# Performance work log

Measured on AMD Instinct MI355X. Metric: run time of the kernel, lower is better.

## Reference

```python
import jax, jax.numpy as jnp
import numpy as np

D_MODEL = 1024
N_HEADS = 16
D_HEAD = D_MODEL // N_HEADS
B, S = 4, 2048
NEG_INF = float('-inf')


def setup_inputs() -> dict:
    key = jax.random.key(0)
    ks = jax.random.split(key, 12)
    sc = 1.0 / np.sqrt(D_MODEL)
    inp = {
        'query': jax.random.normal(ks[0], (B, S, D_MODEL), jnp.float32),
        'key': jax.random.normal(ks[1], (B, S, D_MODEL), jnp.float32),
        'value': jax.random.normal(ks[2], (B, S, D_MODEL), jnp.float32),
        'mask': jnp.ones((B, S), jnp.int32),
        'W_q': jax.random.normal(ks[3], (D_MODEL, D_MODEL), jnp.float32) * sc,
        'b_q': jax.random.normal(ks[4], (D_MODEL,), jnp.float32) * sc,
        'W_k': jax.random.normal(ks[5], (D_MODEL, D_MODEL), jnp.float32) * sc,
        'b_k': jax.random.normal(ks[6], (D_MODEL,), jnp.float32) * sc,
        'W_v': jax.random.normal(ks[7], (D_MODEL, D_MODEL), jnp.float32) * sc,
        'b_v': jax.random.normal(ks[8], (D_MODEL,), jnp.float32) * sc,
        'W_o': jax.random.normal(ks[9], (D_MODEL, D_MODEL), jnp.float32) * sc,
        'b_o': jax.random.normal(ks[10], (D_MODEL,), jnp.float32) * sc,
    }
    return inp


def reference(query, key, value, mask, W_q, b_q, W_k, b_k, W_v, b_v, W_o, b_o):
    b, s, d = query.shape
    # QKV projections, split heads: [B,S,D] -> [B,H,S,Dh]
    def proj(x, W, bias):
        y = x @ W + bias
        return y.reshape(b, s, N_HEADS, D_HEAD).transpose(0, 2, 1, 3)
    q = proj(query, W_q, b_q)
    k = proj(key, W_k, b_k)
    v = proj(value, W_v, b_v)
    # NOTE: original scales by d_head**2 (not sqrt) — kept faithful.
    e = jnp.einsum('bhqd,bhkd->bhqk', q, k) / (D_HEAD ** 2)
    # key padding mask: [B,S] -> additive [B,1,1,S]
    pad = jnp.where(mask == 0, NEG_INF, 0.0).astype(e.dtype)[:, None, None, :]
    e = e + pad
    # causal mask: additive lower-triangular
    causal = jnp.where(jnp.tril(jnp.ones((s, s), bool)), 0.0, NEG_INF).astype(e.dtype)
    e = e + causal[None, None, :, :]
    a = jax.nn.softmax(e, axis=-1)
    c = jnp.einsum('bhqk,bhkd->bhqd', a, v)  # [B,H,S,Dh]
    c = c.transpose(0, 2, 1, 3).reshape(b, s, d)
    return c @ W_o + b_o
```

## Files before the change

### kernel.cpp

```cpp
#include <hip/hip_runtime.h>

typedef __bf16 bf16;
typedef unsigned int u32;
typedef float f32x4 __attribute__((ext_vector_type(4)));
typedef __bf16 bf16x4 __attribute__((ext_vector_type(4)));
typedef __bf16 bf16x8 __attribute__((ext_vector_type(8)));

#define MFMA(a, b, c) __builtin_amdgcn_mfma_f32_16x16x32_bf16((a), (b), (c), 0, 0, 0)

static constexpr int Bc = 4;
static constexpr int Sc = 2048;
static constexpr int Hc = 16;
static constexpr int DHc = 64;
static constexpr int Dc = 1024;
static constexpr int Mc = Bc * Sc;

__device__ __forceinline__ void load_lds16(const bf16* gp, bf16* lp) {
    __builtin_amdgcn_global_load_lds(
        reinterpret_cast<const __attribute__((address_space(1))) u32*>(
            reinterpret_cast<uintptr_t>(gp)),
        reinterpret_cast<__attribute__((address_space(3))) u32*>(
            static_cast<u32>(reinterpret_cast<uintptr_t>(lp))),
        16, 0, 0);
}

__global__ void fill_diag(float* out, int n) {
    int i = blockIdx.x * 256 + threadIdx.x;
    if (i < n) out[i] = 1000.0f;
}

__global__ __launch_bounds__(256) void cvt_bf16(const float* __restrict__ in,
                                                bf16* __restrict__ out, int n) {
    int i = (blockIdx.x * 256 + threadIdx.x) * 8;
    if (i < n) {
        f32x4 a = *(const f32x4*)&in[i];
        f32x4 b = *(const f32x4*)&in[i + 4];
        bf16x8 v;
#pragma unroll
        for (int j = 0; j < 4; ++j) { v[j] = (bf16)a[j]; v[j + 4] = (bf16)b[j]; }
        *(bf16x8*)&out[i] = v;
    }
}

__global__ __launch_bounds__(256) void transpose4(
    const float* __restrict__ A0, const float* __restrict__ A1,
    const float* __restrict__ A2, const float* __restrict__ A3,
    bf16* __restrict__ O0, bf16* __restrict__ O1,
    bf16* __restrict__ O2, bf16* __restrict__ O3) {
    __shared__ bf16 t[32][33];
    const float* in = blockIdx.z == 0 ? A0 : blockIdx.z == 1 ? A1
                    : blockIdx.z == 2 ? A2 : A3;
    bf16* out = blockIdx.z == 0 ? O0 : blockIdx.z == 1 ? O1
              : blockIdx.z == 2 ? O2 : O3;
    int x = blockIdx.x * 32 + threadIdx.x;
#pragma unroll
    for (int j = 0; j < 32; j += 8) {
        int y = blockIdx.y * 32 + threadIdx.y + j;
        t[threadIdx.y + j][threadIdx.x] = (bf16)in[y * 1024 + x];
    }
    __syncthreads();
    int x2 = blockIdx.y * 32 + threadIdx.x;
#pragma unroll
    for (int j = 0; j < 32; j += 8) {
        int y2 = blockIdx.x * 32 + threadIdx.y + j;
        out[y2 * 1024 + x2] = t[threadIdx.x][threadIdx.y + j];
    }
}

template <int MODE, typename TOUT>
__global__ __launch_bounds__(256) void gemm_bt(const bf16* __restrict__ A,
                                               const bf16* __restrict__ Wt,
                                               const float* __restrict__ bias,
                                               TOUT* __restrict__ out,
                                               int M, int N, int K) {
    __shared__ alignas(16) bf16 As[128 * 32];
    __shared__ alignas(16) bf16 Bs[128 * 32];
    const int tid = threadIdx.x;
    const int wave = tid >> 6, lane = tid & 63;
    const int quad = lane >> 4, l16 = lane & 15;
    const int wr = (wave >> 1) * 64, wc = (wave & 1) * 64;
    const int id = blockIdx.y * 8 + blockIdx.x;
    const int sw = (id & 7) * 64 + (id >> 3);
    const int row0 = (sw >> 3) * 128, col0 = (sw & 7) * 128;

    const int sr = wave * 32 + (lane >> 2);
    const int sk = (lane & 3) * 8;
    const bf16* gA = &A[(size_t)(row0 + sr) * K + sk];
    const bf16* gB = &Wt[(size_t)(col0 + sr) * K + sk];
    bf16* lA = &As[wave * 32 * 32];
    bf16* lB = &Bs[wave * 32 * 32];

    f32x4 acc[4][4];
#pragma unroll
    for (int mi = 0; mi < 4; ++mi)
#pragma unroll
        for (int ni = 0; ni < 4; ++ni)
            acc[mi][ni] = (f32x4){0.f, 0.f, 0.f, 0.f};

    for (int k0 = 0; k0 < K; k0 += 32) {
        __syncthreads();
        load_lds16(gA + k0, lA);
        load_lds16(gA + k0 + 16 * K, lA + 16 * 32);
        load_lds16(gB + k0, lB);
        load_lds16(gB + k0 + 16 * K, lB + 16 * 32);
        __syncthreads();

        bf16x8 af[4], bf_[4];
#pragma unroll
        for (int mi = 0; mi < 4; ++mi)
            af[mi] = *(const bf16x8*)&As[(wr + mi * 16 + l16) * 32 + quad * 8];
#pragma unroll
        for (int ni = 0; ni < 4; ++ni)
            bf_[ni] = *(const bf16x8*)&Bs[(wc + ni * 16 + l16) * 32 + quad * 8];
#pragma unroll
        for (int mi = 0; mi < 4; ++mi)
#pragma unroll
            for (int ni = 0; ni < 4; ++ni)
                acc[mi][ni] = MFMA(af[mi], bf_[ni], acc[mi][ni]);
    }

#pragma unroll
    for (int mi = 0; mi < 4; ++mi) {
#pragma unroll
        for (int ni = 0; ni < 4; ++ni) {
            int col = col0 + wc + ni * 16 + l16;
            float bv = bias[col];
#pragma unroll
            for (int r = 0; r < 4; ++r) {
                int row = row0 + wr + mi * 16 + quad * 4 + r;
                float v = acc[mi][ni][r] + bv;
                size_t off;
                if (MODE == 0) {
                    off = (size_t)row * N + col;
                } else {
                    int b = row >> 11, s = row & (Sc - 1);
                    int h = col >> 6, dh = col & (DHc - 1);
                    if (MODE == 1)
                        off = (((size_t)(b * Hc + h) * Sc + s) << 6) + dh;
                    else
                        off = (((size_t)(b * Hc + h) * DHc + dh) << 11) + s;
                }
                out[off] = (TOUT)v;
            }
        }
    }
}

static constexpr int LPP = 72;
static constexpr float CEXP = 1.4426950408889634f / 4096.0f;

__global__ __launch_bounds__(256, 2) void attn_fwd(const bf16* __restrict__ Q,
                                                   const bf16* __restrict__ K,
                                                   const bf16* __restrict__ Vt,
                                                   const int* __restrict__ mask,
                                                   bf16* __restrict__ Ctx) {
    __shared__ alignas(16) bf16 Ks[2][64 * 64];
    __shared__ alignas(16) bf16 Vs[2][64 * 64];
    __shared__ alignas(16) bf16 Ps[4][32 * LPP];
    __shared__ alignas(16) float msk_all[Sc];

    const int tid = threadIdx.x;
    const int wave = tid >> 6, lane = tid & 63;
    const int quad = lane >> 4, l16 = lane & 15;
    const int id = blockIdx.y * 8 + blockIdx.x;
    const int sw = (id & 7) * 64 + (id >> 3);
    const int bh = sw >> 3, p = sw & 7;
    const int b = bh >> 4, h = bh & 15;

    {
        const int i = tid * 8;
        int4 m0 = *(const int4*)&mask[b * Sc + i];
        int4 m1 = *(const int4*)&mask[b * Sc + i + 4];
        f32x4 f0 = {m0.x ? 0.f : -1e30f, m0.y ? 0.f : -1e30f,
                    m0.z ? 0.f : -1e30f, m0.w ? 0.f : -1e30f};
        f32x4 f1 = {m1.x ? 0.f : -1e30f, m1.y ? 0.f : -1e30f,
                    m1.z ? 0.f : -1e30f, m1.w ? 0.f : -1e30f};
        *(f32x4*)&msk_all[i] = f0;
        *(f32x4*)&msk_all[i + 4] = f1;
    }

    const int swz = ((lane & 7) ^ (lane >> 3)) << 4;
    const int rA = wave * 16 + (lane >> 3);
    const char* gK0 = (const char*)K + (size_t)bh * Sc * (DHc * 2)
                    + (size_t)rA * 128 + swz;
    const char* gV0 = (const char*)Vt + (size_t)bh * DHc * (Sc * 2)
                    + (size_t)rA * (Sc * 2) + swz;
    bf16* lK0 = &Ks[0][(wave * 16) * 64];
    bf16* lV0 = &Vs[0][(wave * 16) * 64];

    const int m7 = l16 & 7;
    const int gsw0 = ((0 + quad) ^ m7) * 8;
    const int gsw1 = ((4 + quad) ^ m7) * 8;

#define STAGE(BUF, KB)                                                        \
    do {                                                                      \
        load_lds16((const bf16*)(gK0 + (size_t)(KB) * 128),                   \
                   lK0 + (BUF) * (64 * 64));                                  \
        load_lds16((const bf16*)(gK0 + (size_t)(KB) * 128 + 1024),            \
                   lK0 + (BUF) * (64 * 64) + 8 * 64);                         \
        load_lds16((const bf16*)(gV0 + (size_t)(KB) * 2),                     \
                   lV0 + (BUF) * (64 * 64));                                  \
        load_lds16((const bf16*)(gV0 + (size_t)(KB) * 2 + 8 * 4096),          \
                   lV0 + (BUF) * (64 * 64) + 8 * 64);                         \
    } while (0)

#pragma unroll 1
    for (int pass = 0; pass < 2; ++pass) {
        const int qt = pass ? p : 15 - p;
        const int qr0 = qt * 128 + wave * 32;
        const int qmax = qr0 + 31;

        bf16x8 bq[2][2];
#pragma unroll
        for (int mt = 0; mt < 2; ++mt) {
            const size_t qoff = ((size_t)bh * Sc + qr0 + mt * 16 + l16) * DHc;
            bq[mt][0] = *(const bf16x8*)&Q[qoff + quad * 8];
            bq[mt][1] = *(const bf16x8*)&Q[qoff + 32 + quad * 8];
        }

        f32x4 accO[2][4];
#pragma unroll
        for (int mt = 0; mt < 2; ++mt)
#pragma unroll
            for (int oi = 0; oi < 4; ++oi) accO[mt][oi] = (f32x4){0.f, 0.f, 0.f, 0.f};
        float l_part[2] = {0.f, 0.f};

        const int nkt = 2 * qt + 2;
        STAGE(0, 0);
        __syncthreads();
        int cur = 0;
#pragma unroll 1
        for (int kt = 0; kt < nkt; ++kt) {
            const int kb = kt * 64;
            if (kt + 1 < nkt) STAGE(cur ^ 1, kb + 64);
            if (kb <= qmax) {
                const bf16* Kb_ = &Ks[cur][0];
                const bf16* Vb_ = &Vs[cur][0];

                f32x4 st[2][4];
                __builtin_amdgcn_s_setprio(1);
#pragma unroll
                for (int kti = 0; kti < 4; ++kti) {
                    bf16x8 ak0 = *(const bf16x8*)&Kb_[(kti * 16 + l16) * 64 + gsw0];
                    bf16x8 ak1 = *(const bf16x8*)&Kb_[(kti * 16 + l16) * 64 + gsw1];
#pragma unroll
                    for (int mt = 0; mt < 2; ++mt) {
                        f32x4 z = {0.f, 0.f, 0.f, 0.f};
                        z = MFMA(ak0, bq[mt][0], z);
                        z = MFMA(ak1, bq[mt][1], z);
                        st[mt][kti] = z;
                    }
                }
                __builtin_amdgcn_s_setprio(0);

#define SM_TILE(DIAG)                                                          \
                _Pragma("unroll")                                              \
                for (int mt = 0; mt < 2; ++mt) {                               \
                    _Pragma("unroll")                                          \
                    for (int kti = 0; kti < 4; ++kti) {                        \
                        const f32x4 mkv =                                      \
                            *(const f32x4*)&msk_all[kb + kti * 16 + quad * 4]; \
                        const int cbase =                                      \
                            kb + kti * 16 + quad * 4 - (qr0 + mt * 16);        \
                        bf16x4 pv;                                             \
                        _Pragma("unroll")                                      \
                        for (int r = 0; r < 4; ++r) {                          \
                            float s = st[mt][kti][r] * CEXP + mkv[r];          \
                            if (DIAG) s = (cbase + r > l16) ? -1e30f : s;      \
                            float p_ = __builtin_amdgcn_exp2f(s);              \
                            l_part[mt] += p_;                                  \
                            pv[r] = (bf16)p_;                                  \
                        }                                                      \
                        *(bf16x4*)&Ps[wave][(mt * 16 + l16) * LPP +            \
                                            kti * 16 + quad * 4] = pv;         \
                    }                                                          \
                }
                if (kb + 63 > qr0) { SM_TILE(1) } else { SM_TILE(0) }
#undef SM_TILE

                __builtin_amdgcn_s_setprio(1);
#pragma unroll
                for (int kk = 0; kk < 2; ++kk) {
                    bf16x8 ap0 = *(const bf16x8*)&Ps[wave][(l16) * LPP + kk * 32 + quad * 8];
                    bf16x8 ap1 = *(const bf16x8*)&Ps[wave][(16 + l16) * LPP + kk * 32 + quad * 8];
                    const int vg = kk ? gsw1 : gsw0;
#pragma unroll
                    for (int oi = 0; oi < 4; ++oi) {
                        bf16x8 bv = *(const bf16x8*)&Vb_[(oi * 16 + l16) * 64 + vg];
                        accO[0][oi] = MFMA(ap0, bv, accO[0][oi]);
                        accO[1][oi] = MFMA(ap1, bv, accO[1][oi]);
                    }
                }
                __builtin_amdgcn_s_setprio(0);
            }
            asm volatile("s_waitcnt vmcnt(0)" ::: "memory");
            __builtin_amdgcn_s_barrier();
            __builtin_amdgcn_sched_barrier(0);
            cur ^= 1;
        }

        float lvi[2][4];
#pragma unroll
        for (int mt = 0; mt < 2; ++mt) {
            float l = l_part[mt];
            l += __shfl_xor(l, 16);
            l += __shfl_xor(l, 32);
#pragma unroll
            for (int r = 0; r < 4; ++r)
                lvi[mt][r] = __builtin_amdgcn_rcpf(__shfl(l, quad * 4 + r));
        }
#pragma unroll
        for (int mt = 0; mt < 2; ++mt)
#pragma unroll
            for (int oi = 0; oi < 4; ++oi)
#pragma unroll
                for (int r = 0; r < 4; ++r) {
                    int s = qr0 + mt * 16 + quad * 4 + r;
                    int dh = oi * 16 + l16;
                    float v = accO[mt][oi][r] * lvi[mt][r];
                    Ctx[((size_t)b * Sc + s) * Dc + h * DHc + dh] = (bf16)v;
                }
    }
#undef STAGE
}

extern "C" void kernel_launch(void* const* d_in, const int* in_sizes, int n_in,
                              void* d_out, int out_size, void* d_ws, size_t ws_size,
                              hipStream_t stream) {
    const float* query = (const float*)d_in[0];
    const float* key_i = (const float*)d_in[1];
    const float* value = (const float*)d_in[2];
    const int* mask    = (const int*)d_in[3];
    const float* W_q = (const float*)d_in[4];
    const float* b_q = (const float*)d_in[5];
    const float* W_k = (const float*)d_in[6];
    const float* b_k = (const float*)d_in[7];
    const float* W_v = (const float*)d_in[8];
    const float* b_v = (const float*)d_in[9];
    const float* W_o = (const float*)d_in[10];
    const float* b_o = (const float*)d_in[11];
    float* out = (float*)d_out;

    const size_t MB = 1024 * 1024;
    const size_t NEED = 72 * MB;
    if (ws_size < NEED) {
        fill_diag<<<(out_size + 255) / 256, 256, 0, stream>>>(out, out_size);
        return;
    }

    char* ws = (char*)d_ws;
    bf16* WtQ = (bf16*)(ws + 0 * MB);
    bf16* WtK = (bf16*)(ws + 2 * MB);
    bf16* WtV = (bf16*)(ws + 4 * MB);
    bf16* WtO = (bf16*)(ws + 6 * MB);
    bf16* Xin = (bf16*)(ws + 8 * MB);
    bf16* Ctx = (bf16*)(ws + 8 * MB);
    bf16* Qb  = (bf16*)(ws + 24 * MB);
    bf16* Kb  = (bf16*)(ws + 40 * MB);
    bf16* Vtb = (bf16*)(ws + 56 * MB);

    transpose4<<<dim3(32, 32, 4), dim3(32, 8), 0, stream>>>(
        W_q, W_k, W_v, W_o, WtQ, WtK, WtV, WtO);

    const int ncv = Mc * Dc;
    dim3 gg(Dc / 128, Mc / 128);

    cvt_bf16<<<ncv / (256 * 8), 256, 0, stream>>>(query, Xin, ncv);
    gemm_bt<1, bf16><<<gg, 256, 0, stream>>>(Xin, WtQ, b_q, Qb, Mc, Dc, Dc);
    cvt_bf16<<<ncv / (256 * 8), 256, 0, stream>>>(key_i, Xin, ncv);
    gemm_bt<1, bf16><<<gg, 256, 0, stream>>>(Xin, WtK, b_k, Kb, Mc, Dc, Dc);
    cvt_bf16<<<ncv / (256 * 8), 256, 0, stream>>>(value, Xin, ncv);
    gemm_bt<2, bf16><<<gg, 256, 0, stream>>>(Xin, WtV, b_v, Vtb, Mc, Dc, Dc);

    attn_fwd<<<dim3(8, Bc * Hc), 256, 0, stream>>>(Qb, Kb, Vtb, mask, Ctx);

    gemm_bt<0, float><<<gg, 256, 0, stream>>>(Ctx, WtO, b_o, out, Mc, Dc, Dc);
}
```

Measured before the change: 346.4 us.

## Triple-buffer GEMM LDS tiles with async global-to-LDS prefetch two stages ahead

The projection GEMM now keeps three LDS buffers per operand and issues global_load_lds for tile i+2 while MFMAs run on tile i. Explicit vmcnt waits and one barrier per iteration replace the two __syncthreads around each synchronous load. This is meant to hide global memory latency behind compute. The cost is triple the LDS footprint (48KB per block), which may reduce occupancy.

```diff
diff --git a/kernel.cpp b/kernel.cpp
--- a/kernel.cpp
+++ b/kernel.cpp
@@ -73,8 +73,8 @@
                                                const float* __restrict__ bias,
                                                TOUT* __restrict__ out,
                                                int M, int N, int K) {
-    __shared__ alignas(16) bf16 As[128 * 32];
-    __shared__ alignas(16) bf16 Bs[128 * 32];
+    __shared__ alignas(16) bf16 As[3][128 * 32];
+    __shared__ alignas(16) bf16 Bs[3][128 * 32];
     const int tid = threadIdx.x;
     const int wave = tid >> 6, lane = tid & 63;
     const int quad = lane >> 4, l16 = lane & 15;
@@ -87,8 +87,15 @@
     const int sk = (lane & 3) * 8;
     const bf16* gA = &A[(size_t)(row0 + sr) * K + sk];
     const bf16* gB = &Wt[(size_t)(col0 + sr) * K + sk];
-    bf16* lA = &As[wave * 32 * 32];
-    bf16* lB = &Bs[wave * 32 * 32];
+    const int wo = wave * 32 * 32;
+
+#define GSTAGE(BUF, KOFF)                                                   \
+    do {                                                                    \
+        load_lds16(gA + (KOFF), &As[BUF][wo]);                              \
+        load_lds16(gA + (KOFF) + 16 * K, &As[BUF][wo + 16 * 32]);           \
+        load_lds16(gB + (KOFF), &Bs[BUF][wo]);                              \
+        load_lds16(gB + (KOFF) + 16 * K, &Bs[BUF][wo + 16 * 32]);           \
+    } while (0)
 
     f32x4 acc[4][4];
 #pragma unroll
@@ -97,27 +104,39 @@
         for (int ni = 0; ni < 4; ++ni)
             acc[mi][ni] = (f32x4){0.f, 0.f, 0.f, 0.f};
 
-    for (int k0 = 0; k0 < K; k0 += 32) {
-        __syncthreads();
-        load_lds16(gA + k0, lA);
-        load_lds16(gA + k0 + 16 * K, lA + 16 * 32);
-        load_lds16(gB + k0, lB);
-        load_lds16(gB + k0 + 16 * K, lB + 16 * 32);
-        __syncthreads();
+    const int nk = K / 32;
+    GSTAGE(0, 0);
+    GSTAGE(1, 32);
+    asm volatile("s_waitcnt vmcnt(4)" ::: "memory");
+    __builtin_amdgcn_s_barrier();
+    __builtin_amdgcn_sched_barrier(0);
+
+    int cur = 0, nxt = 2;
+#pragma unroll 1
+    for (int i = 0; i < nk; ++i) {
+        if (i + 2 < nk) GSTAGE(nxt, (i + 2) * 32);
 
         bf16x8 af[4], bf_[4];
 #pragma unroll
         for (int mi = 0; mi < 4; ++mi)
-            af[mi] = *(const bf16x8*)&As[(wr + mi * 16 + l16) * 32 + quad * 8];
+            af[mi] = *(const bf16x8*)&As[cur][(wr + mi * 16 + l16) * 32 + quad * 8];
 #pragma unroll
         for (int ni = 0; ni < 4; ++ni)
-            bf_[ni] = *(const bf16x8*)&Bs[(wc + ni * 16 + l16) * 32 + quad * 8];
+            bf_[ni] = *(const bf16x8*)&Bs[cur][(wc + ni * 16 + l16) * 32 + quad * 8];
 #pragma unroll
         for (int mi = 0; mi < 4; ++mi)
 #pragma unroll
             for (int ni = 0; ni < 4; ++ni)
                 acc[mi][ni] = MFMA(af[mi], bf_[ni], acc[mi][ni]);
-    }
+
+        if (i + 2 < nk) asm volatile("s_waitcnt vmcnt(4)" ::: "memory");
+        else            asm volatile("s_waitcnt vmcnt(0)" ::: "memory");
+        __builtin_amdgcn_s_barrier();
+        __builtin_amdgcn_sched_barrier(0);
+        cur = (cur == 2) ? 0 : cur + 1;
+        nxt = (nxt == 2) ? 0 : nxt + 1;
+    }
+#undef GSTAGE
 
 #pragma unroll
     for (int mi = 0; mi < 4; ++mi) {
```

Result: faster. 319.6 us (-7.7%).
